# Kernel optimization log

Hardware: AMD Instinct MI355X
Metric: run time of the kernel (lower is better)

Reference implementation:

```python
import jax, jax.numpy as jnp
import numpy as np

B, S, D, H = 4, 2048, 1024, 16
DH = D // H  # 64
NEG = -1e9


def setup_inputs() -> dict:
    key = jax.random.key(0)
    k1, k2, k3 = jax.random.split(key, 3)
    x = jax.random.normal(k1, (B, S, D), dtype=jnp.float32)
    w_attn = jax.random.normal(k2, (D, 3 * D), dtype=jnp.float32) * 0.02
    b_attn = jnp.zeros((3 * D,), dtype=jnp.float32)
    w_proj = jax.random.normal(k3, (D, D), dtype=jnp.float32) * 0.02
    b_proj = jnp.zeros((D,), dtype=jnp.float32)
    return {"x": x, "w_attn": w_attn, "b_attn": b_attn, "w_proj": w_proj, "b_proj": b_proj}


def reference(x, w_attn, b_attn, w_proj, b_proj):
    # c_attn: fused QKV projection (Conv1D with rf=1 == dense layer)
    qkv = x @ w_attn + b_attn  # [B,S,3D]
    q, k, v = jnp.split(qkv, 3, axis=-1)

    def split_heads(t):  # [B,S,D] -> [B,H,S,DH]
        return t.reshape(B, S, H, DH).transpose(0, 2, 1, 3)

    q, k, v = split_heads(q), split_heads(k), split_heads(v)

    # scaled scores with additive causal mask (as w*b + -1e9*(1-b))
    w = jnp.einsum("bhqd,bhkd->bhqk", q, k) / jnp.sqrt(jnp.float32(DH))
    causal = jnp.tril(jnp.ones((S, S), dtype=w.dtype))[None, None]
    w = w * causal + NEG * (1.0 - causal)
    w = jax.nn.softmax(w, axis=-1)
    # attn_dropout / resid_dropout: p=0 (eval) -> identity

    a = jnp.einsum("bhqk,bhkd->bhqd", w, v)  # [B,H,S,DH]
    a = a.transpose(0, 2, 1, 3).reshape(B, S, D)  # merge heads
    return a @ w_proj + b_proj
```

## Files before the change

### kernel.cpp

```cpp
#include <hip/hip_runtime.h>


typedef short  s8v   __attribute__((ext_vector_type(8)));
typedef float  f32x4 __attribute__((ext_vector_type(4)));
typedef float  f32x16 __attribute__((ext_vector_type(16)));
typedef unsigned short u16;
typedef u16    u16x4 __attribute__((ext_vector_type(4)));
typedef unsigned int u32;
typedef u32    u32x2 __attribute__((ext_vector_type(2)));

__device__ __forceinline__ u16 f2b(float f) {
  union { float f; unsigned u; } v; v.f = f;
  unsigned r = v.u + 0x7FFFu + ((v.u >> 16) & 1u);
  return (u16)(r >> 16);
}
__device__ __forceinline__ u32 cvtpk(float lo, float hi) {
  u32 r; asm("v_cvt_pk_bf16_f32 %0, %1, %2" : "=v"(r) : "v"(lo), "v"(hi)); return r;
}
__device__ __forceinline__ void plswap(u32 &d, u32 &s) {
  asm volatile("v_permlane32_swap_b32 %0, %1" : "+v"(d), "+v"(s));
}
__device__ __forceinline__ void gll16(const void* g, void* l) {
  __builtin_amdgcn_global_load_lds((const __attribute__((address_space(1))) void*)g,
                                   (__attribute__((address_space(3))) void*)l, 16, 0, 0);
}

#define QSCALE 0.18033688011112042f

__global__ __launch_bounds__(256) void k_cvt(const float* __restrict__ in,
                                             u16* __restrict__ out, int n4) {
  int t = blockIdx.x * 256 + threadIdx.x;
  if (t < n4) {
    f32x4 f = ((const f32x4*)in)[t];
    u16x4 o;
    o[0] = f2b(f[0]); o[1] = f2b(f[1]); o[2] = f2b(f[2]); o[3] = f2b(f[3]);
    ((u16x4*)out)[t] = o;
  }
}

__global__ __launch_bounds__(256) void k_tr(const float* __restrict__ in,
                                            u16* __restrict__ out, int R, int C) {
  __shared__ float tile[32][33];
  int c0 = blockIdx.x * 32, r0 = blockIdx.y * 32;
  int tx = threadIdx.x, ty = threadIdx.y;
#pragma unroll
  for (int j = 0; j < 4; j++)
    tile[ty + j * 8][tx] = in[(size_t)(r0 + ty + j * 8) * C + c0 + tx];
  __syncthreads();
#pragma unroll
  for (int j = 0; j < 4; j++)
    out[(size_t)(c0 + ty + j * 8) * R + r0 + tx] = f2b(tile[tx][ty + j * 8]);
}

template <int EPI>
__global__ __launch_bounds__(256) void k_gemm(
    const u16* __restrict__ A, const u16* __restrict__ Bt,
    const float* __restrict__ bias,
    u16* __restrict__ qb, u16* __restrict__ kb, u16* __restrict__ vb,
    float* __restrict__ outf, int M, int N, int K) {
  __shared__ u16 lA[128 * 32];
  __shared__ u16 lB[128 * 32];
  const int tid = threadIdx.x;
  const int lane = tid & 63, w = tid >> 6;
  const int wr = (w >> 1) * 64, wc = (w & 1) * 64;
  const int lr = lane & 15, lg = lane >> 4;
  const int m0 = blockIdx.y * 128, n0 = blockIdx.x * 128;

  const int crow = lane >> 2;
  const int ccol = (lane & 3) * 8;
  const u16* gA = A + (size_t)(m0 + 32 * w + crow) * K + ccol;
  const u16* gB = Bt + (size_t)(n0 + 32 * w + crow) * K + ccol;

  f32x4 acc[4][4];
  f32x4 zz = {0.f, 0.f, 0.f, 0.f};
#pragma unroll
  for (int m = 0; m < 4; m++)
#pragma unroll
    for (int n = 0; n < 4; n++) acc[m][n] = zz;

  const int nk = K / 32;
  for (int kt = 0; kt < nk; ++kt) {
    gll16(gA + kt * 32, &lA[w * 1024]);
    gll16(gA + kt * 32 + 16 * (size_t)K, &lA[w * 1024 + 512]);
    gll16(gB + kt * 32, &lB[w * 1024]);
    gll16(gB + kt * 32 + 16 * (size_t)K, &lB[w * 1024 + 512]);
    __syncthreads();
    s8v af[4], bf[4];
#pragma unroll
    for (int m = 0; m < 4; m++)
      af[m] = *(const s8v*)&lA[(wr + m * 16 + lr) * 32 + 8 * lg];
#pragma unroll
    for (int n = 0; n < 4; n++)
      bf[n] = *(const s8v*)&lB[(wc + n * 16 + lr) * 32 + 8 * lg];
#pragma unroll
    for (int m = 0; m < 4; m++)
#pragma unroll
      for (int n = 0; n < 4; n++)
        acc[m][n] = __builtin_amdgcn_mfma_f32_16x16x32_bf16(af[m], bf[n], acc[m][n], 0, 0, 0);
    __syncthreads();
  }

#pragma unroll
  for (int m = 0; m < 4; m++) {
#pragma unroll
    for (int n = 0; n < 4; n++) {
      const int col = n0 + wc + n * 16 + lr;
      const float bb = bias[col];
      const int row0 = m0 + wr + m * 16 + 4 * lg;
      if (EPI == 0) {
        const int which = col >> 10, d = col & 1023, h = d >> 6, dh = d & 63;
        if (which == 2) {
          const int b = row0 >> 11, s = row0 & 2047;
          u16x4 ov;
#pragma unroll
          for (int r = 0; r < 4; r++) ov[r] = f2b(acc[m][n][r] + bb);
          *(u16x4*)(vb + ((size_t)((b * 16 + h) * 64 + dh)) * 2048 + s) = ov;
        } else {
          u16* dst = which == 0 ? qb : kb;
          const float sc = which == 0 ? QSCALE : 1.0f;
#pragma unroll
          for (int r = 0; r < 4; r++) {
            const int row = row0 + r;
            const int b = row >> 11, s = row & 2047;
            dst[(size_t)((b * 16 + h) * 2048 + s) * 64 + dh] = f2b((acc[m][n][r] + bb) * sc);
          }
        }
      } else {
#pragma unroll
        for (int r = 0; r < 4; r++)
          outf[(size_t)(row0 + r) * N + col] = acc[m][n][r] + bb;
      }
    }
  }
}

__global__ __launch_bounds__(256, 3) void k_attn(
    const u16* __restrict__ Q, const u16* __restrict__ K,
    const u16* __restrict__ Vt, u16* __restrict__ O) {
  __shared__ u16 lKV[2][8192];
  const int x = blockIdx.x;
  const int bh = ((x & 7) << 3) | ((x >> 3) & 7);
  const int qt = 15 - (x >> 6);
  const int tid = threadIdx.x, lane = tid & 63, w = tid >> 6;
  const int l31 = lane & 31, h = lane >> 5;
  const int qbase = qt * 128 + w * 32;
  const u16* Kb = K + (size_t)bh * 2048 * 64;
  const u16* Vb = Vt + (size_t)bh * 64 * 2048;

  const int skv = tid >> 2;
  const int ssl = (tid & 3) * 2;

  s8v kR0, kR1, vR0, vR1;
  auto pref = [&](int kv0) {
    const u16* gk = Kb + (size_t)(kv0 + skv) * 64 + ssl * 8;
    const u16* gv = Vb + (size_t)skv * 2048 + kv0 + ssl * 8;
    kR0 = *(const s8v*)gk; kR1 = *(const s8v*)(gk + 8);
    vR0 = *(const s8v*)gv; vR1 = *(const s8v*)(gv + 8);
  };
  auto stage = [&](int buf) {
    u16* base = &lKV[buf][0];
    *(s8v*)&base[(ssl * 64 + (skv ^ ssl)) * 8] = kR0;
    *(s8v*)&base[((ssl + 1) * 64 + (skv ^ (ssl + 1))) * 8] = kR1;
    *(s8v*)&base[4096 + (ssl * 64 + (skv ^ ssl)) * 8] = vR0;
    *(s8v*)&base[4096 + ((ssl + 1) * 64 + (skv ^ (ssl + 1))) * 8] = vR1;
  };

  s8v qf[4];
#pragma unroll
  for (int ks = 0; ks < 4; ks++)
    qf[ks] = *(const s8v*)(Q + (size_t)(bh * 2048 + qbase + l31) * 64 + ks * 16 + 8 * h);

  f32x16 accO0, accO1;
#pragma unroll
  for (int i = 0; i < 16; i++) { accO0[i] = 0.f; accO1[i] = 0.f; }
  float mrun = -1e30f, lrun = 0.f;

  const int ntile = 2 * qt + 2;
  pref(0); stage(0);
  if (ntile > 1) pref(64);

  for (int t = 0; t < ntile; ++t) {
    const int kv0 = t * 64;
    __syncthreads();
    const u16* base = &lKV[t & 1][0];

    if (kv0 <= qbase + 31) {
      f32x16 st0, st1;
#pragma unroll
      for (int i = 0; i < 16; i++) { st0[i] = 0.f; st1[i] = 0.f; }
#pragma unroll
      for (int ks = 0; ks < 4; ks++) {
        const int sl = 2 * ks + h;
        s8v a0 = *(const s8v*)&base[(sl * 64 + (l31 ^ sl)) * 8];
        s8v a1 = *(const s8v*)&base[(sl * 64 + ((32 + l31) ^ sl)) * 8];
        st0 = __builtin_amdgcn_mfma_f32_32x32x16_bf16(a0, qf[ks], st0, 0, 0, 0);
        st1 = __builtin_amdgcn_mfma_f32_32x32x16_bf16(a1, qf[ks], st1, 0, 0, 0);
      }
      if (kv0 + 63 > qbase) {
        const int dq = qbase + l31 - kv0;
#pragma unroll
        for (int r = 0; r < 16; r++) {
          const int kl = (r & 3) + 8 * (r >> 2) + 4 * h;
          if (kl > dq) st0[r] = -1e30f;
          if (kl + 32 > dq) st1[r] = -1e30f;
        }
      }
      float mx = st0[0];
#pragma unroll
      for (int r = 1; r < 16; r++) mx = fmaxf(mx, st0[r]);
#pragma unroll
      for (int r = 0; r < 16; r++) mx = fmaxf(mx, st1[r]);
      mx = fmaxf(mx, __shfl_xor(mx, 32));
      if (!__all(mx <= mrun + 11.0f)) {
        const float mnew = fmaxf(mrun, mx);
        const float f = exp2f(mrun - mnew);
        lrun *= f;
#pragma unroll
        for (int r = 0; r < 16; r++) { accO0[r] *= f; accO1[r] *= f; }
        mrun = mnew;
      }
      float s = 0.f;
#pragma unroll
      for (int r = 0; r < 16; r++) { st0[r] = exp2f(st0[r] - mrun); s += st0[r]; }
#pragma unroll
      for (int r = 0; r < 16; r++) { st1[r] = exp2f(st1[r] - mrun); s += st1[r]; }
      s += __shfl_xor(s, 32);
      lrun += s;
      u32 W0[8], W1[8];
#pragma unroll
      for (int a = 0; a < 4; a++) {
        W0[2 * a]     = cvtpk(st0[4 * a], st0[4 * a + 1]);
        W0[2 * a + 1] = cvtpk(st0[4 * a + 2], st0[4 * a + 3]);
        W1[2 * a]     = cvtpk(st1[4 * a], st1[4 * a + 1]);
        W1[2 * a + 1] = cvtpk(st1[4 * a + 2], st1[4 * a + 3]);
      }
#pragma unroll
      for (int ks = 0; ks < 4; ks++) {
        const int kp = ks & 1;
        u32 x0 = (ks < 2) ? W0[4 * kp]     : W1[4 * kp];
        u32 y0 = (ks < 2) ? W0[4 * kp + 2] : W1[4 * kp + 2];
        u32 x1 = (ks < 2) ? W0[4 * kp + 1] : W1[4 * kp + 1];
        u32 y1 = (ks < 2) ? W0[4 * kp + 3] : W1[4 * kp + 3];
        plswap(x0, y0);
        plswap(x1, y1);
        union { u32 u[4]; s8v v; } fb;
        fb.u[0] = x0; fb.u[1] = x1; fb.u[2] = y0; fb.u[3] = y1;
        const int sl = 2 * ks + h;
        s8v va0 = *(const s8v*)&base[4096 + (sl * 64 + (l31 ^ sl)) * 8];
        s8v va1 = *(const s8v*)&base[4096 + (sl * 64 + ((32 + l31) ^ sl)) * 8];
        accO0 = __builtin_amdgcn_mfma_f32_32x32x16_bf16(va0, fb.v, accO0, 0, 0, 0);
        accO1 = __builtin_amdgcn_mfma_f32_32x32x16_bf16(va1, fb.v, accO1, 0, 0, 0);
      }
    }
    if (t + 1 < ntile) {
      stage((t + 1) & 1);
      if (t + 2 < ntile) pref((t + 2) * 64);
    }
  }

  const int b_ = bh >> 4, h_ = bh & 15;
  const float rinv = 1.0f / lrun;
  u16* Ob = O + (size_t)(b_ * 2048 + qbase + l31) * 1024 + h_ * 64;
#pragma unroll
  for (int a = 0; a < 4; a++) {
    u32x2 o0, o1;
    o0[0] = cvtpk(accO0[4 * a] * rinv, accO0[4 * a + 1] * rinv);
    o0[1] = cvtpk(accO0[4 * a + 2] * rinv, accO0[4 * a + 3] * rinv);
    o1[0] = cvtpk(accO1[4 * a] * rinv, accO1[4 * a + 1] * rinv);
    o1[1] = cvtpk(accO1[4 * a + 2] * rinv, accO1[4 * a + 3] * rinv);
    *(u32x2*)(Ob + 8 * a + 4 * h) = o0;
    *(u32x2*)(Ob + 32 + 8 * a + 4 * h) = o1;
  }
}

extern "C" void kernel_launch(void* const* d_in, const int* in_sizes, int n_in,
                              void* d_out, int out_size, void* d_ws, size_t ws_size,
                              hipStream_t stream) {
  const float* x      = (const float*)d_in[0];
  const float* w_attn = (const float*)d_in[1];
  const float* b_attn = (const float*)d_in[2];
  const float* w_proj = (const float*)d_in[3];
  const float* b_proj = (const float*)d_in[4];
  float* out = (float*)d_out;

  u16* ws  = (u16*)d_ws;
  u16* xb  = ws;
  u16* wTa = xb + 8388608;
  u16* wTp = wTa + 3145728;
  u16* qb  = wTp + 1048576;
  u16* kb  = qb + 8388608;
  u16* vb  = kb + 8388608;

  k_cvt<<<8192, 256, 0, stream>>>(x, xb, 2097152);
  k_tr<<<dim3(96, 32), dim3(32, 8), 0, stream>>>(w_attn, wTa, 1024, 3072);
  k_tr<<<dim3(32, 32), dim3(32, 8), 0, stream>>>(w_proj, wTp, 1024, 1024);
  k_gemm<0><<<dim3(24, 64), 256, 0, stream>>>(xb, wTa, b_attn, qb, kb, vb, nullptr, 8192, 3072, 1024);
  k_attn<<<1024, 256, 0, stream>>>(qb, kb, vb, xb);
  k_gemm<1><<<dim3(8, 64), 256, 0, stream>>>(xb, wTp, b_proj, nullptr, nullptr, nullptr, out, 8192, 1024, 1024);
}
```

Baseline: 195.5 us.

## Triple-buffer GEMM LDS loads with swizzle, tile remap, and MFMA priority hints

The GEMM main loop now stages K tiles into three LDS buffers with asynchronous global-to-LDS loads issued two steps ahead. It waits on vmcnt and uses a single barrier per step in place of the previous two-syncthreads load-then-compute loop. LDS columns are XOR-swizzled to reduce bank conflicts, workgroups are remapped across the grid to improve cache locality, and occupancy is hinted at 3 blocks per CU. The attention kernel replaces __syncthreads with an explicit lgkmcnt wait plus barrier and raises wave priority around MFMA blocks. In exchange, the GEMM uses three times the LDS and depends on exact vmcnt counts for correctness.

After: 182.6 us. -6.6%, faster.

```diff
diff --git a/kernel.cpp b/kernel.cpp
--- a/kernel.cpp
+++ b/kernel.cpp
@@ -52,24 +52,62 @@
     out[(size_t)(c0 + ty + j * 8) * R + r0 + tx] = f2b(tile[tx][ty + j * 8]);
 }
 
+__device__ __forceinline__ void gemm_tile(const u16* bA, const u16* bB,
+                                          f32x4 (&acc)[4][4],
+                                          int wr, int wc, int lr, int lg) {
+  s8v af[4], bfr[4];
+#pragma unroll
+  for (int m = 0; m < 4; m++) {
+    const int row = wr + m * 16 + lr;
+    af[m] = *(const s8v*)&bA[row * 32 + (lg ^ ((row >> 1) & 3)) * 8];
+  }
+#pragma unroll
+  for (int n = 0; n < 4; n++) {
+    const int row = wc + n * 16 + lr;
+    bfr[n] = *(const s8v*)&bB[row * 32 + (lg ^ ((row >> 1) & 3)) * 8];
+  }
+  __builtin_amdgcn_s_setprio(1);
+#pragma unroll
+  for (int m = 0; m < 4; m++)
+#pragma unroll
+    for (int n = 0; n < 4; n++)
+      acc[m][n] = __builtin_amdgcn_mfma_f32_16x16x32_bf16(af[m], bfr[n], acc[m][n], 0, 0, 0);
+  __builtin_amdgcn_s_setprio(0);
+}
+
 template <int EPI>
-__global__ __launch_bounds__(256) void k_gemm(
+__global__ __launch_bounds__(256, 3) void k_gemm(
     const u16* __restrict__ A, const u16* __restrict__ Bt,
     const float* __restrict__ bias,
     u16* __restrict__ qb, u16* __restrict__ kb, u16* __restrict__ vb,
     float* __restrict__ outf, int M, int N, int K) {
-  __shared__ u16 lA[128 * 32];
-  __shared__ u16 lB[128 * 32];
+  __shared__ u16 lA[3][4096];
+  __shared__ u16 lB[3][4096];
   const int tid = threadIdx.x;
   const int lane = tid & 63, w = tid >> 6;
   const int wr = (w >> 1) * 64, wc = (w & 1) * 64;
   const int lr = lane & 15, lg = lane >> 4;
-  const int m0 = blockIdx.y * 128, n0 = blockIdx.x * 128;
-
-  const int crow = lane >> 2;
-  const int ccol = (lane & 3) * 8;
-  const u16* gA = A + (size_t)(m0 + 32 * w + crow) * K + ccol;
-  const u16* gB = Bt + (size_t)(n0 + 32 * w + crow) * K + ccol;
+
+  const int nwg = gridDim.x * gridDim.y;
+  const int bid = blockIdx.y * gridDim.x + blockIdx.x;
+  const int swz = (bid & 7) * (nwg >> 3) + (bid >> 3);
+  const int m0 = (swz / gridDim.x) * 128, n0 = (swz % gridDim.x) * 128;
+
+  const int rr = lane >> 2;
+  const int cb = ((lane & 3) ^ ((lane >> 3) & 3)) * 16;
+  const size_t K2 = (size_t)K * 2;
+  const char* gAc = (const char*)A + (size_t)m0 * K2;
+  const char* gBc = (const char*)Bt + (size_t)n0 * K2;
+
+  auto stage = [&](int kt, int buf) {
+    const size_t ko = (size_t)kt * 64 + cb;
+    char* dA = (char*)&lA[buf][0];
+    char* dB = (char*)&lB[buf][0];
+    gll16(gAc + (size_t)(32 * w + rr) * K2 + ko,      dA + (2 * w) * 1024);
+    gll16(gAc + (size_t)(32 * w + 16 + rr) * K2 + ko, dA + (2 * w + 1) * 1024);
+    gll16(gBc + (size_t)(32 * w + rr) * K2 + ko,      dB + (2 * w) * 1024);
+    gll16(gBc + (size_t)(32 * w + 16 + rr) * K2 + ko, dB + (2 * w + 1) * 1024);
+  };
 
   f32x4 acc[4][4];
   f32x4 zz = {0.f, 0.f, 0.f, 0.f};
@@ -79,26 +117,25 @@
     for (int n = 0; n < 4; n++) acc[m][n] = zz;
 
   const int nk = K / 32;
-  for (int kt = 0; kt < nk; ++kt) {
-    gll16(gA + kt * 32, &lA[w * 1024]);
-    gll16(gA + kt * 32 + 16 * (size_t)K, &lA[w * 1024 + 512]);
-    gll16(gB + kt * 32, &lB[w * 1024]);
-    gll16(gB + kt * 32 + 16 * (size_t)K, &lB[w * 1024 + 512]);
-    __syncthreads();
-    s8v af[4], bf[4];
-#pragma unroll
-    for (int m = 0; m < 4; m++)
-      af[m] = *(const s8v*)&lA[(wr + m * 16 + lr) * 32 + 8 * lg];
-#pragma unroll
-    for (int n = 0; n < 4; n++)
-      bf[n] = *(const s8v*)&lB[(wc + n * 16 + lr) * 32 + 8 * lg];
-#pragma unroll
-    for (int m = 0; m < 4; m++)
-#pragma unroll
-      for (int n = 0; n < 4; n++)
-        acc[m][n] = __builtin_amdgcn_mfma_f32_16x16x32_bf16(af[m], bf[n], acc[m][n], 0, 0, 0);
-    __syncthreads();
-  }
+  stage(0, 0);
+  if (nk > 1) stage(1, 1);
+
+#define STEP(T, CB, SB)                                                     \
+  if ((T) < nk) {                                                           \
+    if ((T) + 1 < nk) { asm volatile("s_waitcnt vmcnt(4)" ::: "memory"); }  \
+    else              { asm volatile("s_waitcnt vmcnt(0)" ::: "memory"); }  \
+    __builtin_amdgcn_s_barrier();                                           \
+    __builtin_amdgcn_sched_barrier(0);                                      \
+    if ((T) + 2 < nk) stage((T) + 2, (SB));                                 \
+    gemm_tile(&lA[(CB)][0], &lB[(CB)][0], acc, wr, wc, lr, lg);             \
+  }
+
+  for (int t0 = 0; t0 < nk; t0 += 3) {
+    STEP(t0,     0, 2)
+    STEP(t0 + 1, 1, 0)
+    STEP(t0 + 2, 2, 1)
+  }
+#undef STEP
 
 #pragma unroll
   for (int m = 0; m < 4; m++) {
@@ -181,13 +218,16 @@
 
   for (int t = 0; t < ntile; ++t) {
     const int kv0 = t * 64;
-    __syncthreads();
+    asm volatile("s_waitcnt lgkmcnt(0)" ::: "memory");
+    __builtin_amdgcn_s_barrier();
+    __builtin_amdgcn_sched_barrier(0);
     const u16* base = &lKV[t & 1][0];
 
     if (kv0 <= qbase + 31) {
       f32x16 st0, st1;
 #pragma unroll
       for (int i = 0; i < 16; i++) { st0[i] = 0.f; st1[i] = 0.f; }
+      __builtin_amdgcn_s_setprio(1);
 #pragma unroll
       for (int ks = 0; ks < 4; ks++) {
         const int sl = 2 * ks + h;
@@ -196,6 +236,7 @@
         st0 = __builtin_amdgcn_mfma_f32_32x32x16_bf16(a0, qf[ks], st0, 0, 0, 0);
         st1 = __builtin_amdgcn_mfma_f32_32x32x16_bf16(a1, qf[ks], st1, 0, 0, 0);
       }
+      __builtin_amdgcn_s_setprio(0);
       if (kv0 + 63 > qbase) {
         const int dq = qbase + l31 - kv0;
 #pragma unroll
@@ -234,6 +275,7 @@
         W1[2 * a]     = cvtpk(st1[4 * a], st1[4 * a + 1]);
         W1[2 * a + 1] = cvtpk(st1[4 * a + 2], st1[4 * a + 3]);
       }
+      __builtin_amdgcn_s_setprio(1);
 #pragma unroll
       for (int ks = 0; ks < 4; ks++) {
         const int kp = ks & 1;
@@ -251,6 +293,7 @@
         accO0 = __builtin_amdgcn_mfma_f32_32x32x16_bf16(va0, fb.v, accO0, 0, 0, 0);
         accO1 = __builtin_amdgcn_mfma_f32_32x32x16_bf16(va1, fb.v, accO1, 0, 0, 0);
       }
+      __builtin_amdgcn_s_setprio(0);
     }
     if (t + 1 < ntile) {
       stage((t + 1) & 1);
```
